# Performance work log

Measured on AMD Instinct MI355X. Metric: run time of the kernel, lower is better.

Reference implementation:

```python
import jax, jax.numpy as jnp
import numpy as np

VOCAB, EMB, H = 32000, 512, 1024
B, T = 32, 512


def _glorot(key, shape):
    fan_in, fan_out = shape[0], shape[1]
    lim = np.sqrt(6.0 / (fan_in + fan_out))
    return jax.random.uniform(key, shape, jnp.float32, -lim, lim)


def setup_inputs() -> dict:
    key = jax.random.key(0)
    ks = jax.random.split(key, 12)
    tokens = jax.random.randint(ks[0], (B, T), 0, VOCAB)
    # realistic padding: per-row lengths, mask True for valid prefix
    lengths = jax.random.randint(ks[1], (B,), T // 4, T + 1)
    mask = jnp.arange(T)[None, :] < lengths[:, None]  # [B, T] bool
    emb = jax.random.normal(ks[2], (VOCAB, EMB), jnp.float32) * 0.05
    Wf = _glorot(ks[3], (EMB, 3 * H))
    Uf = _glorot(ks[4], (H, 3 * H))
    bf_in = jnp.zeros((3 * H,), jnp.float32)
    bf_rec = jnp.zeros((3 * H,), jnp.float32)
    Wb = _glorot(ks[5], (EMB, 3 * H))
    Ub = _glorot(ks[6], (H, 3 * H))
    bb_in = jnp.zeros((3 * H,), jnp.float32)
    bb_rec = jnp.zeros((3 * H,), jnp.float32)
    return dict(spanish_tokens=tokens, spanish_token_mask=mask, emb=emb,
                Wf=Wf, Uf=Uf, bf_in=bf_in, bf_rec=bf_rec,
                Wb=Wb, Ub=Ub, bb_in=bb_in, bb_rec=bb_rec)


def _gru_dir(x, mask, W, U, b_in, b_rec, reverse):
    # x: [B,T,E], mask: [B,T] bool. Keras GRU, reset_after=True.
    xs = jnp.swapaxes(x, 0, 1)          # [T,B,E]
    ms = jnp.swapaxes(mask, 0, 1)       # [T,B]
    if reverse:
        xs, ms = xs[::-1], ms[::-1]
    xw = xs @ W + b_in                  # [T,B,3H] precomputed input projections

    def step(h, inp):
        xw_t, m_t = inp
        hu = h @ U + b_rec              # [B,3H]
        xz, xr, xh = jnp.split(xw_t, 3, axis=-1)
        uz, ur, uh = jnp.split(hu, 3, axis=-1)
        z = jax.nn.sigmoid(xz + uz)
        r = jax.nn.sigmoid(xr + ur)
        hh = jnp.tanh(xh + r * uh)
        hn = z * h + (1.0 - z) * hh
        hn = jnp.where(m_t[:, None], hn, h)  # masked steps carry state
        return hn, hn

    h0 = jnp.zeros((x.shape[0], U.shape[0]), x.dtype)
    _, ys = jax.lax.scan(step, h0, (xw, ms))
    if reverse:
        ys = ys[::-1]
    return jnp.swapaxes(ys, 0, 1)       # [B,T,H]


def reference(spanish_tokens, spanish_token_mask, emb, Wf, Uf, bf_in, bf_rec, Wb, Ub, bb_in, bb_rec):
    x = emb[spanish_tokens]             # [B,T,E]
    fwd = _gru_dir(x, spanish_token_mask, Wf, Uf, bf_in, bf_rec, reverse=False)
    bwd = _gru_dir(x, spanish_token_mask, Wb, Ub, bb_in, bb_rec, reverse=True)
    return fwd + bwd                    # merge_mode='sum'
```

## Files before the change

### kernel.cpp

```cpp
#include <hip/hip_runtime.h>
#include <stdint.h>

#define B_    32
#define T_    512
#define H_    1024
#define H3_   3072
#define EMB_  512

typedef __bf16   bf16x8 __attribute__((ext_vector_type(8)));
typedef float    f32x4  __attribute__((ext_vector_type(4)));
typedef uint32_t u32x4  __attribute__((ext_vector_type(4)));

__device__ __forceinline__ uint32_t f2bf_rne_u(float x){
  union { float f; uint32_t u; } v; v.f = x;
  uint32_t u = v.u;
  return (u + 0x7FFFu + ((u >> 16) & 1u)) >> 16;
}
__device__ __forceinline__ float bf2f(uint32_t h16){
  union { uint32_t u; float f; } v; v.u = h16 << 16; return v.f;
}
__device__ __forceinline__ float sigm(float x){ return 1.f / (1.f + __expf(-x)); }
__device__ __forceinline__ float tanh_f(float x){ float e = __expf(2.f * x); return 1.f - 2.f / (e + 1.f); }

__device__ __forceinline__ f32x4 mfma16(bf16x8 a, bf16x8 b, f32x4 c){
  return __builtin_amdgcn_mfma_f32_16x16x32_bf16(a, b, c, 0, 0, 0);
}

__device__ __forceinline__ bf16x8 upk_hi(u32x4 a, u32x4 b){
  u32x4 r;
  r.x = (a.x >> 16) | (a.y & 0xFFFF0000u);
  r.y = (a.z >> 16) | (a.w & 0xFFFF0000u);
  r.z = (b.x >> 16) | (b.y & 0xFFFF0000u);
  r.w = (b.z >> 16) | (b.w & 0xFFFF0000u);
  return __builtin_bit_cast(bf16x8, r);
}
__device__ __forceinline__ bf16x8 upk_lo(u32x4 a, u32x4 b){
  u32x4 r;
  r.x = (a.x & 0xFFFFu) | (a.y << 16);
  r.y = (a.z & 0xFFFFu) | (a.w << 16);
  r.z = (b.x & 0xFFFFu) | (b.y << 16);
  r.w = (b.z & 0xFFFFu) | (b.w << 16);
  return __builtin_bit_cast(bf16x8, r);
}


__global__ void k_emb2bf(const float* __restrict__ src, unsigned short* __restrict__ dst, int n8){
  int i = blockIdx.x * blockDim.x + threadIdx.x;
  if (i >= n8) return;
  const float4* s = (const float4*)src + (size_t)i * 2;
  float4 x = s[0], y = s[1];
  u32x4 o;
  o.x = f2bf_rne_u(x.x) | (f2bf_rne_u(x.y) << 16);
  o.y = f2bf_rne_u(x.z) | (f2bf_rne_u(x.w) << 16);
  o.z = f2bf_rne_u(y.x) | (f2bf_rne_u(y.y) << 16);
  o.w = f2bf_rne_u(y.z) | (f2bf_rne_u(y.w) << 16);
  ((u32x4*)dst)[i] = o;
}

__global__ void k_packW(const float* __restrict__ Wf, const float* __restrict__ Wb,
                        unsigned short* __restrict__ out){
  int idx = blockIdx.x * 256 + threadIdx.x;
  int lane = idx & 63;
  int ks   = (idx >> 6) & 15;
  int rest = idx >> 10;
  int p  = rest % 3;
  int ct = (rest / 3) & 63;
  int d  = rest / 192;
  const float* W = d ? Wb : Wf;
  int colg = p * 1024 + ct * 16 + (lane & 15);
  int k0   = ks * 32 + ((lane >> 4) << 3);
  unsigned short* o = out + (size_t)idx * 8;
  #pragma unroll
  for (int b = 0; b < 8; ++b)
    o[b] = (unsigned short)f2bf_rne_u(W[(size_t)(k0 + b) * H3_ + colg]);
}

__global__ void k_packU(const float* __restrict__ Uf, const float* __restrict__ Ub,
                        unsigned short* __restrict__ ohi, unsigned short* __restrict__ olo){
  int idx = blockIdx.x * 256 + threadIdx.x;
  int lane = idx & 63;
  int ks   = (idx >> 6) & 31;
  int rest = idx >> 11;
  int p  = rest % 3;
  int ct = (rest / 3) & 63;
  int d  = rest / 192;
  const float* U = d ? Ub : Uf;
  int colg = p * 1024 + ct * 16 + (lane & 15);
  int k0   = ks * 32 + ((lane >> 4) << 3);
  size_t o = (size_t)idx * 8;
  #pragma unroll
  for (int b = 0; b < 8; ++b){
    float u = U[(size_t)(k0 + b) * H3_ + colg];
    uint32_t hi = f2bf_rne_u(u);
    float lo = u - bf2f(hi);
    ohi[o + b] = (unsigned short)hi;
    olo[o + b] = (unsigned short)f2bf_rne_u(lo);
  }
}

__global__ void k_add(float* __restrict__ out, const float* __restrict__ add, int n4){
  int i = blockIdx.x * blockDim.x + threadIdx.x;
  if (i >= n4) return;
  f32x4 a = ((const f32x4*)out)[i];
  f32x4 b = ((const f32x4*)add)[i];
  ((f32x4*)out)[i] = a + b;
}


#define KOUT 8

__global__ __launch_bounds__(256, 1)
void k_gru(const int* __restrict__ tokens,
           const unsigned char* __restrict__ maskp,
           const unsigned short* __restrict__ embb,
           const unsigned short* __restrict__ WF,
           const unsigned short* __restrict__ UFhi,
           const unsigned short* __restrict__ UFlo,
           const float* __restrict__ bin_f, const float* __restrict__ brec_f,
           const float* __restrict__ bin_b, const float* __restrict__ brec_b,
           uint32_t* __restrict__ hpack,
           uint32_t* flags,
           float* out_f, float* out_b, int atomic_out)
{
  const int blk  = blockIdx.x;
  const int d    = blk >> 7;
  const int rg   = (blk >> 6) & 1;
  const int ct   = blk & 63;
  const int chain = d * 2 + rg;
  const int tid  = threadIdx.x;
  const int lane = tid & 63;
  const int wave = tid >> 6;
  const int l15  = lane & 15;
  const int lg   = lane >> 4;
  const int mask_is32 = (maskp[1] == 0) ? 1 : 0;

  const float* bin  = d ? bin_b  : bin_f;
  const float* brec = d ? brec_b : brec_f;
  const int col = ct * 16 + l15;
  const float bz  = bin[col]          + brec[col];
  const float br  = bin[H_ + col]     + brec[H_ + col];
  const float bhx = bin[2 * H_ + col];
  const float bhu = brec[2 * H_ + col];

  bf16x8 Uh[3][8], Ul[3][8], Wr[3][4];
  {
    const size_t bu = (size_t)(d * 64 + ct) * (3 * 32 * 64 * 8);
    #pragma unroll
    for (int p = 0; p < 3; ++p)
      #pragma unroll
      for (int ks = 0; ks < 8; ++ks){
        size_t off = bu + ((size_t)(p * 32 + (wave * 8 + ks)) * 64 + lane) * 8;
        Uh[p][ks] = *(const bf16x8*)(UFhi + off);
        Ul[p][ks] = *(const bf16x8*)(UFlo + off);
      }
    const size_t bw = (size_t)(d * 64 + ct) * (3 * 16 * 64 * 8);
    #pragma unroll
    for (int p = 0; p < 3; ++p)
      #pragma unroll
      for (int ks = 0; ks < 4; ++ks){
        size_t off = bw + ((size_t)(p * 16 + (wave * 4 + ks)) * 64 + lane) * 8;
        Wr[p][ks] = *(const bf16x8*)(WF + off);
      }
  }

  __shared__ f32x4 red[2][4][4][64];

  uint32_t* hp  = hpack + (size_t)chain * 2 * 16 * H_;
  uint32_t* cnt = flags + chain * 128;
  float* outp = atomic_out ? out_f : (d ? out_b : out_f);

  const f32x4 z4 = {0.f, 0.f, 0.f, 0.f};
  float hreg[4] = {0.f, 0.f, 0.f, 0.f};
  float obuf[KOUT][4];

  for (int tb = 0; tb < T_ / KOUT; ++tb){
    #pragma unroll
    for (int ti = 0; ti < KOUT; ++ti){
      const int t   = tb * KOUT + ti;
      const int par = ti & 1;
      const int te  = d ? (T_ - 1 - t) : t;
      const uint32_t* hcur = hp + (size_t)(t & 1) * 16 * H_;
      uint32_t*       hnxt = hp + (size_t)((t + 1) & 1) * 16 * H_;

      bool mb[4] = {false, false, false, false};
      if (wave == 0){
        #pragma unroll
        for (int i = 0; i < 4; ++i){
          const int row = rg * 16 + (lg << 2) + i;
          const int midx = row * T_ + te;
          mb[i] = mask_is32 ? (((const int*)maskp)[midx] != 0) : (maskp[midx] != 0);
        }
      }

      f32x4 accz = z4, accr = z4, acchx = z4, acchu = z4;

      const int tok0 = tokens[(rg * 16 + l15) * T_ + te];
      #pragma unroll
      for (int ks = 0; ks < 4; ++ks){
        const int koff = (wave * 4 + ks) * 32 + (lg << 3);
        bf16x8 xa0 = *(const bf16x8*)(embb + (size_t)tok0 * EMB_ + koff);
        accz  = mfma16(xa0, Wr[0][ks], accz);
        accr  = mfma16(xa0, Wr[1][ks], accr);
        acchx = mfma16(xa0, Wr[2][ks], acchx);
      }

      if (t > 0){
        if (lane < 4){
          const uint32_t tgt = (uint32_t)(16 * t);
          while (__hip_atomic_load(cnt + lane * 32, __ATOMIC_RELAXED, __HIP_MEMORY_SCOPE_AGENT) < tgt)
            __builtin_amdgcn_s_sleep(1);
        }
      }

      const uint32_t* a0 = hcur + (size_t)l15 * H_ + wave * 256 + (lg << 3);
      u32x4 e0[8], e1[8];

      asm volatile("s_waitcnt vmcnt(0)" ::: "memory");
      __builtin_amdgcn_sched_barrier(0);

      asm volatile(
        "global_load_dwordx4 %0, %8, off sc1\n\t"
        "global_load_dwordx4 %1, %8, off offset:16 sc1\n\t"
        "global_load_dwordx4 %2, %8, off offset:128 sc1\n\t"
        "global_load_dwordx4 %3, %8, off offset:144 sc1\n\t"
        "global_load_dwordx4 %4, %8, off offset:256 sc1\n\t"
        "global_load_dwordx4 %5, %8, off offset:272 sc1\n\t"
        "global_load_dwordx4 %6, %8, off offset:384 sc1\n\t"
        "global_load_dwordx4 %7, %8, off offset:400 sc1\n\t"
        : "=&v"(e0[0]), "=&v"(e0[1]), "=&v"(e0[2]), "=&v"(e0[3]),
          "=&v"(e0[4]), "=&v"(e0[5]), "=&v"(e0[6]), "=&v"(e0[7])
        : "v"(a0));
      asm volatile(
        "global_load_dwordx4 %0, %8, off offset:512 sc1\n\t"
        "global_load_dwordx4 %1, %8, off offset:528 sc1\n\t"
        "global_load_dwordx4 %2, %8, off offset:640 sc1\n\t"
        "global_load_dwordx4 %3, %8, off offset:656 sc1\n\t"
        "global_load_dwordx4 %4, %8, off offset:768 sc1\n\t"
        "global_load_dwordx4 %5, %8, off offset:784 sc1\n\t"
        "global_load_dwordx4 %6, %8, off offset:896 sc1\n\t"
        "global_load_dwordx4 %7, %8, off offset:912 sc1\n\t"
        : "=&v"(e1[0]), "=&v"(e1[1]), "=&v"(e1[2]), "=&v"(e1[3]),
          "=&v"(e1[4]), "=&v"(e1[5]), "=&v"(e1[6]), "=&v"(e1[7])
        : "v"(a0));

      asm volatile("s_waitcnt vmcnt(8)" ::: "memory");
      __builtin_amdgcn_sched_barrier(0);
      #pragma unroll
      for (int ks2 = 0; ks2 < 4; ++ks2){
        bf16x8 h0 = upk_hi(e0[2*ks2], e0[2*ks2+1]);
        bf16x8 L0 = upk_lo(e0[2*ks2], e0[2*ks2+1]);
        #pragma unroll
        for (int p = 0; p < 3; ++p){
          f32x4* acc = (p == 0) ? &accz : (p == 1) ? &accr : &acchu;
          *acc = mfma16(h0, Uh[p][ks2], *acc);
          *acc = mfma16(L0, Uh[p][ks2], *acc);
          *acc = mfma16(h0, Ul[p][ks2], *acc);
        }
      }
      asm volatile("s_waitcnt vmcnt(0)" ::: "memory");
      __builtin_amdgcn_sched_barrier(0);
      #pragma unroll
      for (int ks2 = 0; ks2 < 4; ++ks2){
        const int ks = 4 + ks2;
        bf16x8 h0 = upk_hi(e1[2*ks2], e1[2*ks2+1]);
        bf16x8 L0 = upk_lo(e1[2*ks2], e1[2*ks2+1]);
        #pragma unroll
        for (int p = 0; p < 3; ++p){
          f32x4* acc = (p == 0) ? &accz : (p == 1) ? &accr : &acchu;
          *acc = mfma16(h0, Uh[p][ks], *acc);
          *acc = mfma16(L0, Uh[p][ks], *acc);
          *acc = mfma16(h0, Ul[p][ks], *acc);
        }
      }

      red[par][wave][0][lane] = accz;
      red[par][wave][1][lane] = accr;
      red[par][wave][2][lane] = acchx;
      red[par][wave][3][lane] = acchu;
      __syncthreads();

      if (wave == 0){
        f32x4 rz  = red[par][0][0][lane] + red[par][1][0][lane] + red[par][2][0][lane] + red[par][3][0][lane];
        f32x4 rr  = red[par][0][1][lane] + red[par][1][1][lane] + red[par][2][1][lane] + red[par][3][1][lane];
        f32x4 rhx = red[par][0][2][lane] + red[par][1][2][lane] + red[par][2][2][lane] + red[par][3][2][lane];
        f32x4 rhu = red[par][0][3][lane] + red[par][1][3][lane] + red[par][2][3][lane] + red[par][3][3][lane];
        #pragma unroll
        for (int i = 0; i < 4; ++i){
          const int row = (lg << 2) + i;
          const float z  = sigm(rz[i] + bz);
          const float r  = sigm(rr[i] + br);
          const float hh = tanh_f(rhx[i] + bhx + r * (rhu[i] + bhu));
          const float hprev = hreg[i];
          const float v = mb[i] ? (z * hprev + (1.f - z) * hh) : hprev;
          hreg[i] = v;
          obuf[ti][i] = v;
          const uint32_t hi = f2bf_rne_u(v);
          const float lo = v - bf2f(hi);
          __hip_atomic_store(hnxt + (size_t)row * H_ + col, (hi << 16) | f2bf_rne_u(lo),
                             __ATOMIC_RELAXED, __HIP_MEMORY_SCOPE_AGENT);
        }
        asm volatile("s_waitcnt vmcnt(0)" ::: "memory");
        if (tid == 0)
          atomicAdd(cnt + (ct & 3) * 32, 1u);

        if (ti == KOUT - 1){
          #pragma unroll
          for (int j = 0; j < KOUT; ++j){
            const int tj  = tb * KOUT + j;
            const int tej = d ? (T_ - 1 - tj) : tj;
            #pragma unroll
            for (int i = 0; i < 4; ++i){
              const int row = rg * 16 + (lg << 2) + i;
              const size_t oidx = ((size_t)row * T_ + tej) * H_ + col;
              if (atomic_out) atomicAdd(outp + oidx, obuf[j][i]);
              else            outp[oidx] = obuf[j][i];
            }
          }
        }
      }
    }
  }
}


extern "C" void kernel_launch(void* const* d_in, const int* in_sizes, int n_in,
                              void* d_out, int out_size, void* d_ws, size_t ws_size,
                              hipStream_t stream) {
  const int*   tokens = (const int*)d_in[0];
  const unsigned char* mask = (const unsigned char*)d_in[1];
  const float* emb   = (const float*)d_in[2];
  const float* Wf    = (const float*)d_in[3];
  const float* Uf    = (const float*)d_in[4];
  const float* bfin  = (const float*)d_in[5];
  const float* bfrec = (const float*)d_in[6];
  const float* Wb    = (const float*)d_in[7];
  const float* Ub    = (const float*)d_in[8];
  const float* bbin  = (const float*)d_in[9];
  const float* bbrec = (const float*)d_in[10];
  float* out = (float*)d_out;
  char*  ws  = (char*)d_ws;

  const size_t o_embb  = 0;
  const size_t o_wf    = 32768000;
  const size_t o_ufhi  = 39059456;
  const size_t o_uflo  = 51642368;
  const size_t o_hpack = 64225280;
  const size_t o_flags = 64749568;
  const size_t o_bwd   = 64751616;
  const size_t need_full = o_bwd + 67108864;

  const int atomic_mode = (ws_size < need_full) ? 1 : 0;

  hipMemsetAsync(ws + o_hpack, 0, 524288 + 2048, stream);

  k_emb2bf<<<8000, 256, 0, stream>>>(emb, (unsigned short*)(ws + o_embb), 2048000);
  k_packW <<<1536, 256, 0, stream>>>(Wf, Wb, (unsigned short*)(ws + o_wf));
  k_packU <<<3072, 256, 0, stream>>>(Uf, Ub, (unsigned short*)(ws + o_ufhi),
                                             (unsigned short*)(ws + o_uflo));
  if (atomic_mode)
    hipMemsetAsync(out, 0, (size_t)out_size * sizeof(float), stream);

  k_gru<<<256, 256, 0, stream>>>(tokens, mask,
                                 (const unsigned short*)(ws + o_embb),
                                 (const unsigned short*)(ws + o_wf),
                                 (const unsigned short*)(ws + o_ufhi),
                                 (const unsigned short*)(ws + o_uflo),
                                 bfin, bfrec, bbin, bbrec,
                                 (uint32_t*)(ws + o_hpack),
                                 (uint32_t*)(ws + o_flags),
                                 out, (float*)(ws + o_bwd), atomic_mode);

  if (!atomic_mode)
    k_add<<<16384, 256, 0, stream>>>(out, (const float*)(ws + o_bwd), 4194304);
}
```

Before: 3.204 ms.

## Triple-buffer hidden state, per-wave flag waits, split accumulators for finer load overlap

Moves the hidden-state exchange from double to triple buffering, so a fast block can publish step t+1 while slower blocks are still reading step t-1's buffer. This removes the write-after-read hazard that double buffering left unguarded. Each wave now spins on only the counter covering its own K-slice. Counters are regrouped by ct>>4 so each counter tracks a contiguous 256-column range. The recurrent MFMA chain is split into two independent accumulator sets, and the h loads are consumed in four vmcnt stages instead of two to overlap loads with math and shorten dependency chains. The cost is extra workspace and more registers.

```diff
diff --git a/kernel.cpp b/kernel.cpp
--- a/kernel.cpp
+++ b/kernel.cpp
@@ -108,6 +108,20 @@
 
 
 #define KOUT 8
+
+#define HPROC(PA, PB, KS, G0, G1, G2) do { \
+  bf16x8 hh_ = upk_hi(PA, PB); \
+  bf16x8 hl_ = upk_lo(PA, PB); \
+  G0 = mfma16(hh_, Uh[0][KS], G0); \
+  G0 = mfma16(hl_, Uh[0][KS], G0); \
+  G0 = mfma16(hh_, Ul[0][KS], G0); \
+  G1 = mfma16(hh_, Uh[1][KS], G1); \
+  G1 = mfma16(hl_, Uh[1][KS], G1); \
+  G1 = mfma16(hh_, Ul[1][KS], G1); \
+  G2 = mfma16(hh_, Uh[2][KS], G2); \
+  G2 = mfma16(hl_, Uh[2][KS], G2); \
+  G2 = mfma16(hh_, Ul[2][KS], G2); \
+} while(0)
 
 __global__ __launch_bounds__(256, 1)
 void k_gru(const int* __restrict__ tokens,
@@ -165,13 +179,15 @@
 
   __shared__ f32x4 red[2][4][4][64];
 
-  uint32_t* hp  = hpack + (size_t)chain * 2 * 16 * H_;
+  uint32_t* hp  = hpack + (size_t)chain * 3 * 16 * H_;
   uint32_t* cnt = flags + chain * 128;
   float* outp = atomic_out ? out_f : (d ? out_b : out_f);
 
   const f32x4 z4 = {0.f, 0.f, 0.f, 0.f};
   float hreg[4] = {0.f, 0.f, 0.f, 0.f};
   float obuf[KOUT][4];
+
+  int bcur = 0, bnxt = 1;
 
   for (int tb = 0; tb < T_ / KOUT; ++tb){
     #pragma unroll
@@ -179,8 +195,8 @@
       const int t   = tb * KOUT + ti;
       const int par = ti & 1;
       const int te  = d ? (T_ - 1 - t) : t;
-      const uint32_t* hcur = hp + (size_t)(t & 1) * 16 * H_;
-      uint32_t*       hnxt = hp + (size_t)((t + 1) & 1) * 16 * H_;
+      const uint32_t* hcur = hp + (size_t)bcur * 16 * H_;
+      uint32_t*       hnxt = hp + (size_t)bnxt * 16 * H_;
 
       bool mb[4] = {false, false, false, false};
       if (wave == 0){
@@ -192,31 +208,28 @@
         }
       }
 
-      f32x4 accz = z4, accr = z4, acchx = z4, acchu = z4;
-
+      f32x4 ax0 = z4, ax1 = z4, ax2 = z4;
       const int tok0 = tokens[(rg * 16 + l15) * T_ + te];
       #pragma unroll
       for (int ks = 0; ks < 4; ++ks){
         const int koff = (wave * 4 + ks) * 32 + (lg << 3);
         bf16x8 xa0 = *(const bf16x8*)(embb + (size_t)tok0 * EMB_ + koff);
-        accz  = mfma16(xa0, Wr[0][ks], accz);
-        accr  = mfma16(xa0, Wr[1][ks], accr);
-        acchx = mfma16(xa0, Wr[2][ks], acchx);
-      }
-
-      if (t > 0){
-        if (lane < 4){
-          const uint32_t tgt = (uint32_t)(16 * t);
-          while (__hip_atomic_load(cnt + lane * 32, __ATOMIC_RELAXED, __HIP_MEMORY_SCOPE_AGENT) < tgt)
-            __builtin_amdgcn_s_sleep(1);
-        }
+        ax0 = mfma16(xa0, Wr[0][ks], ax0);
+        ax1 = mfma16(xa0, Wr[1][ks], ax1);
+        ax2 = mfma16(xa0, Wr[2][ks], ax2);
+      }
+
+      asm volatile("s_waitcnt vmcnt(0)" ::: "memory");
+      __builtin_amdgcn_sched_barrier(0);
+
+      if (t > 0 && lane == 0){
+        const uint32_t tgt = (uint32_t)(16 * t);
+        while (__hip_atomic_load(cnt + wave * 32, __ATOMIC_RELAXED, __HIP_MEMORY_SCOPE_AGENT) < tgt)
+          __builtin_amdgcn_s_sleep(1);
       }
 
       const uint32_t* a0 = hcur + (size_t)l15 * H_ + wave * 256 + (lg << 3);
       u32x4 e0[8], e1[8];
-
-      asm volatile("s_waitcnt vmcnt(0)" ::: "memory");
-      __builtin_amdgcn_sched_barrier(0);
 
       asm volatile(
         "global_load_dwordx4 %0, %8, off sc1\n\t"
@@ -243,40 +256,29 @@
           "=&v"(e1[4]), "=&v"(e1[5]), "=&v"(e1[6]), "=&v"(e1[7])
         : "v"(a0));
 
+      f32x4 zA = z4, zB = z4, rA = z4, rB = z4, uA = z4, uB = z4;
+
+      asm volatile("s_waitcnt vmcnt(12)" ::: "memory");
+      __builtin_amdgcn_sched_barrier(0);
+      HPROC(e0[0], e0[1], 0, zA, rA, uA);
+      HPROC(e0[2], e0[3], 1, zB, rB, uB);
       asm volatile("s_waitcnt vmcnt(8)" ::: "memory");
       __builtin_amdgcn_sched_barrier(0);
-      #pragma unroll
-      for (int ks2 = 0; ks2 < 4; ++ks2){
-        bf16x8 h0 = upk_hi(e0[2*ks2], e0[2*ks2+1]);
-        bf16x8 L0 = upk_lo(e0[2*ks2], e0[2*ks2+1]);
-        #pragma unroll
-        for (int p = 0; p < 3; ++p){
-          f32x4* acc = (p == 0) ? &accz : (p == 1) ? &accr : &acchu;
-          *acc = mfma16(h0, Uh[p][ks2], *acc);
-          *acc = mfma16(L0, Uh[p][ks2], *acc);
-          *acc = mfma16(h0, Ul[p][ks2], *acc);
-        }
-      }
+      HPROC(e0[4], e0[5], 2, zA, rA, uA);
+      HPROC(e0[6], e0[7], 3, zB, rB, uB);
+      asm volatile("s_waitcnt vmcnt(4)" ::: "memory");
+      __builtin_amdgcn_sched_barrier(0);
+      HPROC(e1[0], e1[1], 4, zA, rA, uA);
+      HPROC(e1[2], e1[3], 5, zB, rB, uB);
       asm volatile("s_waitcnt vmcnt(0)" ::: "memory");
       __builtin_amdgcn_sched_barrier(0);
-      #pragma unroll
-      for (int ks2 = 0; ks2 < 4; ++ks2){
-        const int ks = 4 + ks2;
-        bf16x8 h0 = upk_hi(e1[2*ks2], e1[2*ks2+1]);
-        bf16x8 L0 = upk_lo(e1[2*ks2], e1[2*ks2+1]);
-        #pragma unroll
-        for (int p = 0; p < 3; ++p){
-          f32x4* acc = (p == 0) ? &accz : (p == 1) ? &accr : &acchu;
-          *acc = mfma16(h0, Uh[p][ks], *acc);
-          *acc = mfma16(L0, Uh[p][ks], *acc);
-          *acc = mfma16(h0, Ul[p][ks], *acc);
-        }
-      }
-
-      red[par][wave][0][lane] = accz;
-      red[par][wave][1][lane] = accr;
-      red[par][wave][2][lane] = acchx;
-      red[par][wave][3][lane] = acchu;
+      HPROC(e1[4], e1[5], 6, zA, rA, uA);
+      HPROC(e1[6], e1[7], 7, zB, rB, uB);
+
+      red[par][wave][0][lane] = ax0 + zA + zB;
+      red[par][wave][1][lane] = ax1 + rA + rB;
+      red[par][wave][2][lane] = ax2;
+      red[par][wave][3][lane] = uA + uB;
       __syncthreads();
 
       if (wave == 0){
@@ -301,7 +303,7 @@
         }
         asm volatile("s_waitcnt vmcnt(0)" ::: "memory");
         if (tid == 0)
-          atomicAdd(cnt + (ct & 3) * 32, 1u);
+          atomicAdd(cnt + (ct >> 4) * 32, 1u);
 
         if (ti == KOUT - 1){
           #pragma unroll
@@ -318,6 +320,10 @@
           }
         }
       }
+
+      const int bt = bnxt + 1;
+      bcur = bnxt;
+      bnxt = (bt == 3) ? 0 : bt;
     }
   }
 }
@@ -345,13 +351,13 @@
   const size_t o_ufhi  = 39059456;
   const size_t o_uflo  = 51642368;
   const size_t o_hpack = 64225280;
-  const size_t o_flags = 64749568;
-  const size_t o_bwd   = 64751616;
+  const size_t o_flags = 65011712;
+  const size_t o_bwd   = 65013760;
   const size_t need_full = o_bwd + 67108864;
 
   const int atomic_mode = (ws_size < need_full) ? 1 : 0;
 
-  hipMemsetAsync(ws + o_hpack, 0, 524288 + 2048, stream);
+  hipMemsetAsync(ws + o_hpack, 0, 786432 + 2048, stream);
 
   k_emb2bf<<<8000, 256, 0, stream>>>(emb, (unsigned short*)(ws + o_embb), 2048000);
   k_packW <<<1536, 256, 0, stream>>>(Wf, Wb, (unsigned short*)(ws + o_wf));
```

New measurement: 3.250 ms. Within noise of the previous version (+1.4%).
